# Optimization experiments

Measured on AMD Instinct MI355X. Metric: run time of the kernel, lower is better.

## Reference

```python
import jax, jax.numpy as jnp
import numpy as np
from math import sqrt


def setup_inputs() -> dict:
    key = jax.random.key(0)
    kq, kk, kv = jax.random.split(key, 3)
    B, L, S, H, E, D = 2, 4096, 4096, 8, 64, 64
    queries = jax.random.normal(kq, (B, L, H, E), dtype=jnp.float32)
    keys = jax.random.normal(kk, (B, S, H, E), dtype=jnp.float32)
    values = jax.random.normal(kv, (B, S, H, D), dtype=jnp.float32)
    attn_mask = jnp.zeros((1,), dtype=bool)  # unused (mask_flag=False)
    return {"queries": queries, "keys": keys, "values": values, "attn_mask": attn_mask}


def reference(queries, keys, values, attn_mask):
    # queries: [B,L,H,E], keys: [B,S,H,E], values: [B,S,H,D]
    E = queries.shape[-1]
    scale = 1.0 / sqrt(E)
    # log-domain value preprocessing: exp(V - max_over_seq(V))
    value_max = jnp.max(values, axis=1, keepdims=True)  # [B,1,H,D]
    v_exp = jnp.exp(values - value_max)                 # [B,S,H,D]
    # standard QK^T softmax (mask_flag=False, dropout=0 in eval)
    scores = jnp.einsum('blhe,bshe->bhls', queries, keys)  # [B,H,L,S]
    A = jax.nn.softmax(scale * scores, axis=-1)
    V = jnp.einsum('bhls,bshd->blhd', A, v_exp)            # [B,L,H,D]
    # log-domain postprocessing: log(AV) + value_max (broadcasts over L)
    V = jnp.log(V) + value_max
    return V
```

## Files before the change

kernel.cpp:

```cpp
#include <hip/hip_runtime.h>
#include <math.h>

#define NB 2
#define NL 4096
#define NS 4096
#define NH 8
#define NE 64
#define ND 64
#define SB 64
#define NT (NS / SB)
#define GT (NT / 2)
#define TILE_B 8192
#define LOG2E 1.4426950408889634f
#define SC2 (0.125f * LOG2E)

typedef __attribute__((ext_vector_type(8))) short bf16x8;
typedef __attribute__((ext_vector_type(4))) float f32x4;
typedef __attribute__((ext_vector_type(16))) float f32x16;
typedef unsigned short ushort_t;

__device__ __forceinline__ short f2bf(float f) {
  union { float f; unsigned u; } v; v.f = f;
  unsigned u = v.u;
  return (short)((u + 0x7fffu + ((u >> 16) & 1u)) >> 16);
}

__device__ __forceinline__ unsigned cvt_pk_bf16(float lo, float hi) {
  unsigned r;
  asm("v_cvt_pk_bf16_f32 %0, %1, %2" : "=v"(r) : "v"(lo), "v"(hi));
  return r;
}

__device__ __forceinline__ void gload16(const void* g, void* l) {
  __builtin_amdgcn_global_load_lds(
      (const __attribute__((address_space(1))) void*)g,
      (__attribute__((address_space(3))) void*)l, 16, 0, 0);
}


__global__ __launch_bounds__(256) void kvprep(const float* __restrict__ Kg,
                                              const float* __restrict__ Vg,
                                              ushort_t* __restrict__ kimg,
                                              ushort_t* __restrict__ vimg) {
  int blk = blockIdx.x;
  int bh = blk >> 6, tile = blk & 63;
  int b = bh >> 3, h = bh & 7;
  int t = threadIdx.x;
  int srow = t >> 2, c16 = (t & 3) * 16;
  {
    const float4* p4 =
        (const float4*)(Kg + (((size_t)b * NS + tile * SB + srow) * NH + h) * NE + c16);
    float4 a = p4[0], bq = p4[1], c = p4[2], d = p4[3];
    unsigned u0 = cvt_pk_bf16(a.x, a.y), u1 = cvt_pk_bf16(a.z, a.w);
    unsigned u2 = cvt_pk_bf16(bq.x, bq.y), u3 = cvt_pk_bf16(bq.z, bq.w);
    unsigned u4 = cvt_pk_bf16(c.x, c.y), u5 = cvt_pk_bf16(c.z, c.w);
    unsigned u6 = cvt_pk_bf16(d.x, d.y), u7 = cvt_pk_bf16(d.z, d.w);
    char* base = (char*)kimg + (size_t)blk * TILE_B;
    int off0 = (c16 >> 4) * 2048 + (srow >> 5) * 1024 + (srow & 31) * 16;
    uint4 w0 = {u0, u1, u2, u3}, w1 = {u4, u5, u6, u7};
    *(uint4*)(base + off0) = w0;
    *(uint4*)(base + off0 + 512) = w1;
  }
  {
    __shared__ short Vsh[64 * 72];
    const float4* p4 =
        (const float4*)(Vg + (((size_t)b * NS + tile * SB + srow) * NH + h) * ND + c16);
    float4 va = p4[0], vb = p4[1], vc = p4[2], vd = p4[3];
    float fv[16] = {va.x, va.y, va.z, va.w, vb.x, vb.y, vb.z, vb.w,
                    vc.x, vc.y, vc.z, vc.w, vd.x, vd.y, vd.z, vd.w};
#pragma unroll
    for (int i = 0; i < 16; ++i)
      Vsh[(c16 + i) * 72 + srow] = f2bf(__expf(fv[i]));
    __syncthreads();
    int dr = t >> 2, sc = (t & 3) * 16;
    bf16x8 o0 = *(const bf16x8*)&Vsh[dr * 72 + sc];
    bf16x8 o1 = *(const bf16x8*)&Vsh[dr * 72 + sc + 8];
    char* base = (char*)vimg + (size_t)blk * TILE_B;
    int off0 = (sc >> 4) * 2048 + (dr >> 5) * 1024 + (dr & 31) * 16;
    *(bf16x8*)(base + off0) = o0;
    *(bf16x8*)(base + off0 + 512) = o1;
  }
}

__global__ __launch_bounds__(512) void laser_fast(
    const float* __restrict__ Qg, const ushort_t* __restrict__ Kimg,
    const ushort_t* __restrict__ Vimg, float* __restrict__ Og) {
  int orig = blockIdx.x;
  int bid = (orig & 7) * 64 + (orig >> 3);
  int qt = bid & 31;
  int bh = bid >> 5;
  int b = bh >> 3, hh = bh & 7;
  int t = threadIdx.x;
  int w = t >> 6;
  int grp = w >> 2;
  int wi = w & 3;
  int lane = t & 63;
  int lq = lane & 31;
  int h = lane >> 5;

  __shared__ __attribute__((aligned(16))) char smem[65536];
  char* kls = smem + grp * 16384;
  char* vls = smem + 32768 + grp * 16384;

  const char* kbase = (const char*)Kimg + (size_t)bh * (NT * TILE_B);
  const char* vbase = (const char*)Vimg + (size_t)bh * (NT * TILE_B);

  int q0 = qt * 128 + wi * 32;
  const float* qp = Qg + (((size_t)b * NL + q0 + lq) * NH + hh) * NE;
  bf16x8 qf[4];
#pragma unroll
  for (int kk = 0; kk < 4; ++kk) {
    int e0 = 16 * kk + 8 * h;
    float4 x = *(const float4*)(qp + e0);
    float4 y = *(const float4*)(qp + e0 + 4);
    union { bf16x8 v; unsigned u[4]; } tm;
    tm.u[0] = cvt_pk_bf16(x.x * SC2, x.y * SC2);
    tm.u[1] = cvt_pk_bf16(x.z * SC2, x.w * SC2);
    tm.u[2] = cvt_pk_bf16(y.x * SC2, y.y * SC2);
    tm.u[3] = cvt_pk_bf16(y.z * SC2, y.w * SC2);
    qf[kk] = tm.v;
  }

  f32x16 acc0, acc1;
  float l_r = 0.f;
#pragma unroll
  for (int i = 0; i < 16; ++i) { acc0[i] = 0.f; acc1[i] = 0.f; }

  int soff = wi * 2048 + lane * 16;
  int tbase = grp * GT;
  int fb = h * 512 + lq * 16;

#define STAGE(buf, ti)                                                       \
  do {                                                                       \
    const char* ks = kbase + (size_t)(tbase + (ti)) * TILE_B + soff;         \
    const char* vs = vbase + (size_t)(tbase + (ti)) * TILE_B + soff;         \
    gload16(ks, kls + (buf) * 8192 + wi * 2048);                             \
    gload16(ks + 1024, kls + (buf) * 8192 + wi * 2048 + 1024);               \
    gload16(vs, vls + (buf) * 8192 + wi * 2048);                             \
    gload16(vs + 1024, vls + (buf) * 8192 + wi * 2048 + 1024);               \
  } while (0)

#define MAKE_PA(P, g, idx)                                                   \
    do {                                                                     \
      unsigned a0 = cvt_pk_bf16(P[8 * (g) + 0], P[8 * (g) + 1]);             \
      unsigned a1 = cvt_pk_bf16(P[8 * (g) + 2], P[8 * (g) + 3]);             \
      unsigned b0 = cvt_pk_bf16(P[8 * (g) + 4], P[8 * (g) + 5]);             \
      unsigned b1 = cvt_pk_bf16(P[8 * (g) + 6], P[8 * (g) + 7]);             \
      auto w02 = __builtin_amdgcn_permlane32_swap(a0, b0, false, false);     \
      auto w13 = __builtin_amdgcn_permlane32_swap(a1, b1, false, false);     \
      union { bf16x8 v; unsigned u[4]; } tm;                                 \
      tm.u[0] = w02[0]; tm.u[1] = w13[0]; tm.u[2] = w02[1]; tm.u[3] = w13[1];\
      pa[idx] = tm.v;                                                        \
    } while (0)

#define COMPUTE(curb)                                                        \
  do {                                                                       \
    const char* Kc = kls + (curb) * 8192;                                    \
    const char* Vc = vls + (curb) * 8192;                                    \
    f32x16 s0, s1;                                                           \
    _Pragma("unroll")                                                        \
    for (int i = 0; i < 16; ++i) { s0[i] = 0.f; s1[i] = 0.f; }               \
    __builtin_amdgcn_s_setprio(1);                                           \
    _Pragma("unroll")                                                        \
    for (int kk = 0; kk < 4; ++kk) {                                         \
      bf16x8 ka = *(const bf16x8*)(Kc + fb + kk * 2048);                     \
      bf16x8 kb = *(const bf16x8*)(Kc + fb + kk * 2048 + 1024);              \
      s0 = __builtin_amdgcn_mfma_f32_32x32x16_bf16(ka, qf[kk], s0, 0, 0, 0); \
      s1 = __builtin_amdgcn_mfma_f32_32x32x16_bf16(kb, qf[kk], s1, 0, 0, 0); \
    }                                                                        \
    __builtin_amdgcn_s_setprio(0);                                           \
    _Pragma("unroll")                                                        \
    for (int i = 0; i < 16; ++i) {                                           \
      s0[i] = __builtin_amdgcn_exp2f(s0[i]);                                 \
      s1[i] = __builtin_amdgcn_exp2f(s1[i]);                                 \
    }                                                                        \
    {                                                                        \
      float t0 = (s0[0] + s0[1]) + (s0[2] + s0[3]);                          \
      float t1 = (s0[4] + s0[5]) + (s0[6] + s0[7]);                          \
      float t2 = (s0[8] + s0[9]) + (s0[10] + s0[11]);                        \
      float t3 = (s0[12] + s0[13]) + (s0[14] + s0[15]);                      \
      float t4 = (s1[0] + s1[1]) + (s1[2] + s1[3]);                          \
      float t5 = (s1[4] + s1[5]) + (s1[6] + s1[7]);                          \
      float t6 = (s1[8] + s1[9]) + (s1[10] + s1[11]);                        \
      float t7 = (s1[12] + s1[13]) + (s1[14] + s1[15]);                      \
      l_r += ((t0 + t1) + (t2 + t3)) + ((t4 + t5) + (t6 + t7));              \
    }                                                                        \
    bf16x8 pa[4];                                                            \
    MAKE_PA(s0, 0, 0);                                                       \
    MAKE_PA(s0, 1, 1);                                                       \
    MAKE_PA(s1, 0, 2);                                                       \
    MAKE_PA(s1, 1, 3);                                                       \
    __builtin_amdgcn_s_setprio(1);                                           \
    _Pragma("unroll")                                                        \
    for (int kk = 0; kk < 4; ++kk) {                                         \
      bf16x8 v0 = *(const bf16x8*)(Vc + fb + kk * 2048);                     \
      bf16x8 v1 = *(const bf16x8*)(Vc + fb + kk * 2048 + 1024);              \
      acc0 = __builtin_amdgcn_mfma_f32_32x32x16_bf16(pa[kk], v0, acc0, 0, 0, 0); \
      acc1 = __builtin_amdgcn_mfma_f32_32x32x16_bf16(pa[kk], v1, acc1, 0, 0, 0); \
    }                                                                        \
    __builtin_amdgcn_s_setprio(0);                                           \
  } while (0)

  STAGE(0, 0);
  int cur = 0;
  for (int ti = 0; ti < GT - 1; ++ti) {
    STAGE(cur ^ 1, ti + 1);
    asm volatile("s_waitcnt vmcnt(4)" ::: "memory");
    __builtin_amdgcn_s_barrier();
    COMPUTE(cur);
    asm volatile("s_waitcnt lgkmcnt(0)" ::: "memory");
    __builtin_amdgcn_s_barrier();
    cur ^= 1;
  }
  asm volatile("s_waitcnt vmcnt(0)" ::: "memory");
  __builtin_amdgcn_s_barrier();
  COMPUTE(cur);
#undef STAGE
#undef MAKE_PA
#undef COMPUTE

  __syncthreads();
  float* exch = (float*)(void*)smem;
  float* lex  = (float*)(void*)(smem + 32768);
  float* lsm  = (float*)(void*)(smem + 33792);
  if (grp == 1) {
    float* e = exch + wi * 2048 + lane;
#pragma unroll
    for (int r = 0; r < 16; ++r) {
      e[r * 64] = acc0[r];
      e[(16 + r) * 64] = acc1[r];
    }
    lex[wi * 64 + lane] = l_r;
  }
  __syncthreads();
  if (grp == 0) {
    float* e = exch + wi * 2048 + lane;
#pragma unroll
    for (int r = 0; r < 16; ++r) {
      acc0[r] += e[r * 64];
      acc1[r] += e[(16 + r) * 64];
    }
    l_r += lex[wi * 64 + lane];

    union { float f; unsigned u; } cu;
    cu.f = l_r;
    auto mm = __builtin_amdgcn_permlane32_swap(cu.u, cu.u, false, false);
    union { unsigned u; float f; } m0, m1;
    m0.u = mm[0]; m1.u = mm[1];
    lsm[wi * 32 + lq] = m0.f + m1.f;

#pragma unroll
    for (int r = 0; r < 16; ++r) {
      int q = (r & 3) + 8 * (r >> 2) + 4 * h;
      float logl = __logf(lsm[wi * 32 + q]);
      size_t o = (((size_t)b * NL + q0 + q) * NH + hh) * ND + lq;
      Og[o] = __logf(acc0[r]) - logl;
      Og[o + 32] = __logf(acc1[r]) - logl;
    }
  }
}

__global__ void vmax_partial(const float* __restrict__ Vp, float* __restrict__ part) {
  int blk = blockIdx.x;
  int bh = blk >> 4, ck = blk & 15;
  int b = bh >> 3, h = bh & 7;
  int t = threadIdx.x;
  int d = t & 63, g = t >> 6;
  const float* base = Vp + (((size_t)b * NS + ck * 256) * NH + h) * ND + d;
  float m = -INFINITY;
  for (int s = g; s < 256; s += 4)
    m = fmaxf(m, base[(size_t)s * NH * ND]);
  __shared__ float red[4][64];
  red[g][d] = m;
  __syncthreads();
  if (t < 64)
    part[(size_t)blk * 64 + t] =
        fmaxf(fmaxf(red[0][t], red[1][t]), fmaxf(red[2][t], red[3][t]));
}

__global__ void vmax_reduce(const float* __restrict__ part, float* __restrict__ vmax) {
  int bh = blockIdx.x, t = threadIdx.x;
  float m = -INFINITY;
#pragma unroll
  for (int c = 0; c < 16; ++c)
    m = fmaxf(m, part[((size_t)bh * 16 + c) * 64 + t]);
  vmax[bh * 64 + t] = m;
}

__global__ __launch_bounds__(256) void laser_slow(
    const float* __restrict__ Qg, const float* __restrict__ Kg,
    const float* __restrict__ Vg, const float* __restrict__ vmax,
    float* __restrict__ Og) {
  int bid = blockIdx.x;
  int qt = bid & 63;
  int bh = bid >> 6;
  int b = bh >> 3, h = bh & 7;
  int t = threadIdx.x;
  int w = t >> 6;
  int lane = t & 63;
  int lr = lane & 15;
  int lg = lane >> 4;

  __shared__ short Kt[SB * NE];
  __shared__ short Vt[ND * SB];
  __shared__ short Pl[4][16 * SB];
  __shared__ float vmx[ND];

  if (t < ND) vmx[t] = vmax[bh * ND + t];

  int q0 = qt * 64;
  int qrow = q0 + w * 16 + lr;
  const float* qptr = Qg + (((size_t)b * NL + qrow) * NH + h) * NE;
  bf16x8 qf[2];
#pragma unroll
  for (int kf = 0; kf < 2; ++kf) {
    const float4* p4 = (const float4*)(qptr + kf * 32 + lg * 8);
    float4 a = p4[0], bq = p4[1];
    qf[kf][0] = f2bf(a.x);  qf[kf][1] = f2bf(a.y);
    qf[kf][2] = f2bf(a.z);  qf[kf][3] = f2bf(a.w);
    qf[kf][4] = f2bf(bq.x); qf[kf][5] = f2bf(bq.y);
    qf[kf][6] = f2bf(bq.z); qf[kf][7] = f2bf(bq.w);
  }

  f32x4 acc_o[4];
  float m_r[4], l_r[4];
  const f32x4 fzero = {0.f, 0.f, 0.f, 0.f};
#pragma unroll
  for (int i = 0; i < 4; ++i) { acc_o[i] = fzero; m_r[i] = -INFINITY; l_r[i] = 0.f; }

  const float scale = 0.125f;
  int srow = t >> 2;
  int c16 = (t & 3) * 16;

  for (int s0 = 0; s0 < NS; s0 += SB) {
    __syncthreads();
    {
      const float4* kp4 =
          (const float4*)(Kg + (((size_t)b * NS + (s0 + srow)) * NH + h) * NE + c16);
      float4 t0 = kp4[0], t1 = kp4[1], t2 = kp4[2], t3 = kp4[3];
      bf16x8 c0, c1;
      c0[0] = f2bf(t0.x); c0[1] = f2bf(t0.y); c0[2] = f2bf(t0.z); c0[3] = f2bf(t0.w);
      c0[4] = f2bf(t1.x); c0[5] = f2bf(t1.y); c0[6] = f2bf(t1.z); c0[7] = f2bf(t1.w);
      c1[0] = f2bf(t2.x); c1[1] = f2bf(t2.y); c1[2] = f2bf(t2.z); c1[3] = f2bf(t2.w);
      c1[4] = f2bf(t3.x); c1[5] = f2bf(t3.y); c1[6] = f2bf(t3.z); c1[7] = f2bf(t3.w);
      int base = srow * 128 + c16 * 2;
      int swz = (srow & 7) << 4;
      *(bf16x8*)((char*)Kt + ((base) ^ swz)) = c0;
      *(bf16x8*)((char*)Kt + ((base + 16) ^ swz)) = c1;
    }
    {
      const float4* vp4 =
          (const float4*)(Vg + (((size_t)b * NS + (s0 + srow)) * NH + h) * ND + c16);
      float4 t0 = vp4[0], t1 = vp4[1], t2 = vp4[2], t3 = vp4[3];
      float fv[16] = {t0.x, t0.y, t0.z, t0.w, t1.x, t1.y, t1.z, t1.w,
                      t2.x, t2.y, t2.z, t2.w, t3.x, t3.y, t3.z, t3.w};
#pragma unroll
      for (int i = 0; i < 16; ++i) {
        int d = c16 + i;
        int byte = (d * 128 + srow * 2) ^ ((d & 7) << 4);
        *(short*)((char*)Vt + byte) = f2bf(__expf(fv[i] - vmx[d]));
      }
    }
    __syncthreads();

    f32x4 sacc[4];
#pragma unroll
    for (int jt = 0; jt < 4; ++jt) sacc[jt] = fzero;
#pragma unroll
    for (int jt = 0; jt < 4; ++jt) {
      int srw = jt * 16 + lr;
      int rb = srw * 128;
      int swz = (srw & 7) << 4;
      bf16x8 kb0 = *(const bf16x8*)((const char*)Kt + ((rb + lg * 16) ^ swz));
      bf16x8 kb1 = *(const bf16x8*)((const char*)Kt + ((rb + 64 + lg * 16) ^ swz));
      sacc[jt] = __builtin_amdgcn_mfma_f32_16x16x32_bf16(qf[0], kb0, sacc[jt], 0, 0, 0);
      sacc[jt] = __builtin_amdgcn_mfma_f32_16x16x32_bf16(qf[1], kb1, sacc[jt], 0, 0, 0);
    }

    float mnew[4], corr[4];
#pragma unroll
    for (int r = 0; r < 4; ++r) {
      float x = fmaxf(fmaxf(sacc[0][r], sacc[1][r]),
                      fmaxf(sacc[2][r], sacc[3][r])) * scale;
      x = fmaxf(x, __shfl_xor(x, 1));
      x = fmaxf(x, __shfl_xor(x, 2));
      x = fmaxf(x, __shfl_xor(x, 4));
      x = fmaxf(x, __shfl_xor(x, 8));
      mnew[r] = fmaxf(m_r[r], x);
      corr[r] = __expf(m_r[r] - mnew[r]);
    }
    float rs[4] = {0.f, 0.f, 0.f, 0.f};
    short pb[4][4];
#pragma unroll
    for (int jt = 0; jt < 4; ++jt)
#pragma unroll
      for (int r = 0; r < 4; ++r) {
        float p = __expf(sacc[jt][r] * scale - mnew[r]);
        rs[r] += p;
        pb[jt][r] = f2bf(p);
      }
#pragma unroll
    for (int r = 0; r < 4; ++r) {
      float x = rs[r];
      x += __shfl_xor(x, 1);
      x += __shfl_xor(x, 2);
      x += __shfl_xor(x, 4);
      x += __shfl_xor(x, 8);
      l_r[r] = l_r[r] * corr[r] + x;
      m_r[r] = mnew[r];
    }
    short* pwv = &Pl[w][0];
#pragma unroll
    for (int jt = 0; jt < 4; ++jt)
#pragma unroll
      for (int r = 0; r < 4; ++r) {
        int row = lg * 4 + r, col = jt * 16 + lr;
        int byte = (row * 128 + col * 2) ^ ((row & 7) << 4);
        *(short*)((char*)pwv + byte) = pb[jt][r];
      }
#pragma unroll
    for (int dt = 0; dt < 4; ++dt)
#pragma unroll
      for (int r = 0; r < 4; ++r) acc_o[dt][r] *= corr[r];
#pragma unroll
    for (int kf = 0; kf < 2; ++kf) {
      int ab = lr * 128;
      int aswz = (lr & 7) << 4;
      bf16x8 pa = *(const bf16x8*)((const char*)pwv + ((ab + kf * 64 + lg * 16) ^ aswz));
#pragma unroll
      for (int dt = 0; dt < 4; ++dt) {
        int drow = dt * 16 + lr;
        int vb_byte = (drow * 128 + kf * 64 + lg * 16) ^ ((drow & 7) << 4);
        bf16x8 vb = *(const bf16x8*)((const char*)Vt + vb_byte);
        acc_o[dt] = __builtin_amdgcn_mfma_f32_16x16x32_bf16(pa, vb, acc_o[dt], 0, 0, 0);
      }
    }
  }

#pragma unroll
  for (int r = 0; r < 4; ++r) {
    int row = q0 + w * 16 + lg * 4 + r;
    float logl = __logf(l_r[r]);
#pragma unroll
    for (int dt = 0; dt < 4; ++dt) {
      int d = dt * 16 + lr;
      Og[(((size_t)b * NL + row) * NH + h) * ND + d] =
          __logf(acc_o[dt][r]) - logl + vmx[d];
    }
  }
}

extern "C" void kernel_launch(void* const* d_in, const int* in_sizes, int n_in,
                              void* d_out, int out_size, void* d_ws, size_t ws_size,
                              hipStream_t stream) {
  (void)in_sizes; (void)n_in; (void)out_size;
  const float* Q = (const float*)d_in[0];
  const float* K = (const float*)d_in[1];
  const float* V = (const float*)d_in[2];
  float* out = (float*)d_out;

  float* vmax = (float*)d_ws;
  float* part = (float*)((char*)d_ws + 4096);
  const size_t kimg_off = 1u << 20;
  const size_t vimg_off = (size_t)9u << 20;
  const size_t img_bytes = (size_t)16 * NT * TILE_B;
  bool fast = ws_size >= vimg_off + img_bytes;

  if (fast) {
    ushort_t* kimg = (ushort_t*)((char*)d_ws + kimg_off);
    ushort_t* vimg = (ushort_t*)((char*)d_ws + vimg_off);
    kvprep<<<dim3(1024), dim3(256), 0, stream>>>(K, V, kimg, vimg);
    laser_fast<<<dim3(512), dim3(512), 0, stream>>>(Q, kimg, vimg, out);
  } else {
    vmax_partial<<<dim3(256), dim3(256), 0, stream>>>(V, part);
    vmax_reduce<<<dim3(16), dim3(64), 0, stream>>>(part, vmax);
    laser_slow<<<dim3(1024), dim3(256), 0, stream>>>(Q, K, V, vmax, out);
  }
}
```

Before: 92.69 us.

## Process two 32-query tiles per wave to reuse K/V tiles across queries

Each wave now handles 64 queries instead of 32, so a block covers 256 queries and the grid shrinks from 512 to 256 blocks. K fragments are loaded into registers once and fed to two sets of QK MFMAs, and V fragments are read for both PV accumulations, halving LDS/global K/V traffic per query. This doubles the accumulator and score register footprint. With only 256 blocks on a 256-CU device, occupancy and load balance may suffer. The exchange buffer grows past 64KB of LDS, which may limit residency despite the launch_bounds hint of 2.

```diff
diff --git a/kernel.cpp b/kernel.cpp
--- a/kernel.cpp
+++ b/kernel.cpp
@@ -82,13 +82,13 @@
   }
 }
 
-__global__ __launch_bounds__(512) void laser_fast(
+__global__ __launch_bounds__(512, 2) void laser_fast(
     const float* __restrict__ Qg, const ushort_t* __restrict__ Kimg,
     const ushort_t* __restrict__ Vimg, float* __restrict__ Og) {
   int orig = blockIdx.x;
-  int bid = (orig & 7) * 64 + (orig >> 3);
-  int qt = bid & 31;
-  int bh = bid >> 5;
+  int bid = (orig & 7) * 32 + (orig >> 3);
+  int qt = bid & 15;
+  int bh = bid >> 4;
   int b = bh >> 3, hh = bh & 7;
   int t = threadIdx.x;
   int w = t >> 6;
@@ -98,33 +98,43 @@
   int lq = lane & 31;
   int h = lane >> 5;
 
-  __shared__ __attribute__((aligned(16))) char smem[65536];
+  __shared__ __attribute__((aligned(16))) char smem[68608];
   char* kls = smem + grp * 16384;
   char* vls = smem + 32768 + grp * 16384;
 
   const char* kbase = (const char*)Kimg + (size_t)bh * (NT * TILE_B);
   const char* vbase = (const char*)Vimg + (size_t)bh * (NT * TILE_B);
 
-  int q0 = qt * 128 + wi * 32;
-  const float* qp = Qg + (((size_t)b * NL + q0 + lq) * NH + hh) * NE;
-  bf16x8 qf[4];
+  int q0 = qt * 256 + wi * 64;
+  const float* qpa = Qg + (((size_t)b * NL + q0 + lq) * NH + hh) * NE;
+  const float* qpb = Qg + (((size_t)b * NL + q0 + 32 + lq) * NH + hh) * NE;
+  bf16x8 qfa[4], qfb[4];
 #pragma unroll
   for (int kk = 0; kk < 4; ++kk) {
     int e0 = 16 * kk + 8 * h;
-    float4 x = *(const float4*)(qp + e0);
-    float4 y = *(const float4*)(qp + e0 + 4);
+    float4 x = *(const float4*)(qpa + e0);
+    float4 y = *(const float4*)(qpa + e0 + 4);
     union { bf16x8 v; unsigned u[4]; } tm;
     tm.u[0] = cvt_pk_bf16(x.x * SC2, x.y * SC2);
     tm.u[1] = cvt_pk_bf16(x.z * SC2, x.w * SC2);
     tm.u[2] = cvt_pk_bf16(y.x * SC2, y.y * SC2);
     tm.u[3] = cvt_pk_bf16(y.z * SC2, y.w * SC2);
-    qf[kk] = tm.v;
-  }
-
-  f32x16 acc0, acc1;
-  float l_r = 0.f;
-#pragma unroll
-  for (int i = 0; i < 16; ++i) { acc0[i] = 0.f; acc1[i] = 0.f; }
+    qfa[kk] = tm.v;
+    float4 x2 = *(const float4*)(qpb + e0);
+    float4 y2 = *(const float4*)(qpb + e0 + 4);
+    tm.u[0] = cvt_pk_bf16(x2.x * SC2, x2.y * SC2);
+    tm.u[1] = cvt_pk_bf16(x2.z * SC2, x2.w * SC2);
+    tm.u[2] = cvt_pk_bf16(y2.x * SC2, y2.y * SC2);
+    tm.u[3] = cvt_pk_bf16(y2.z * SC2, y2.w * SC2);
+    qfb[kk] = tm.v;
+  }
+
+  f32x16 acca0, acca1, accb0, accb1;
+  float l_a = 0.f, l_b = 0.f;
+#pragma unroll
+  for (int i = 0; i < 16; ++i) {
+    acca0[i] = 0.f; acca1[i] = 0.f; accb0[i] = 0.f; accb1[i] = 0.f;
+  }
 
   int soff = wi * 2048 + lane * 16;
   int tbase = grp * GT;
@@ -140,33 +150,83 @@
     gload16(vs + 1024, vls + (buf) * 8192 + wi * 2048 + 1024);               \
   } while (0)
 
-#define MAKE_PA(P, g, idx)                                                   \
+#define MAKE_PA(P0, P1)                                                      \
     do {                                                                     \
-      unsigned a0 = cvt_pk_bf16(P[8 * (g) + 0], P[8 * (g) + 1]);             \
-      unsigned a1 = cvt_pk_bf16(P[8 * (g) + 2], P[8 * (g) + 3]);             \
-      unsigned b0 = cvt_pk_bf16(P[8 * (g) + 4], P[8 * (g) + 5]);             \
-      unsigned b1 = cvt_pk_bf16(P[8 * (g) + 6], P[8 * (g) + 7]);             \
-      auto w02 = __builtin_amdgcn_permlane32_swap(a0, b0, false, false);     \
-      auto w13 = __builtin_amdgcn_permlane32_swap(a1, b1, false, false);     \
-      union { bf16x8 v; unsigned u[4]; } tm;                                 \
-      tm.u[0] = w02[0]; tm.u[1] = w13[0]; tm.u[2] = w02[1]; tm.u[3] = w13[1];\
-      pa[idx] = tm.v;                                                        \
+      unsigned a0, a1, b0, b1;                                               \
+      a0 = cvt_pk_bf16(P0[0], P0[1]); a1 = cvt_pk_bf16(P0[2], P0[3]);        \
+      b0 = cvt_pk_bf16(P0[4], P0[5]); b1 = cvt_pk_bf16(P0[6], P0[7]);        \
+      {                                                                      \
+        auto w02 = __builtin_amdgcn_permlane32_swap(a0, b0, false, false);   \
+        auto w13 = __builtin_amdgcn_permlane32_swap(a1, b1, false, false);   \
+        union { bf16x8 v; unsigned u[4]; } tm;                               \
+        tm.u[0] = w02[0]; tm.u[1] = w13[0]; tm.u[2] = w02[1]; tm.u[3] = w13[1]; \
+        pa[0] = tm.v;                                                        \
+      }                                                                      \
+      a0 = cvt_pk_bf16(P0[8], P0[9]);   a1 = cvt_pk_bf16(P0[10], P0[11]);    \
+      b0 = cvt_pk_bf16(P0[12], P0[13]); b1 = cvt_pk_bf16(P0[14], P0[15]);    \
+      {                                                                      \
+        auto w02 = __builtin_amdgcn_permlane32_swap(a0, b0, false, false);   \
+        auto w13 = __builtin_amdgcn_permlane32_swap(a1, b1, false, false);   \
+        union { bf16x8 v; unsigned u[4]; } tm;                               \
+        tm.u[0] = w02[0]; tm.u[1] = w13[0]; tm.u[2] = w02[1]; tm.u[3] = w13[1]; \
+        pa[1] = tm.v;                                                        \
+      }                                                                      \
+      a0 = cvt_pk_bf16(P1[0], P1[1]); a1 = cvt_pk_bf16(P1[2], P1[3]);        \
+      b0 = cvt_pk_bf16(P1[4], P1[5]); b1 = cvt_pk_bf16(P1[6], P1[7]);        \
+      {                                                                      \
+        auto w02 = __builtin_amdgcn_permlane32_swap(a0, b0, false, false);   \
+        auto w13 = __builtin_amdgcn_permlane32_swap(a1, b1, false, false);   \
+        union { bf16x8 v; unsigned u[4]; } tm;                               \
+        tm.u[0] = w02[0]; tm.u[1] = w13[0]; tm.u[2] = w02[1]; tm.u[3] = w13[1]; \
+        pa[2] = tm.v;                                                        \
+      }                                                                      \
+      a0 = cvt_pk_bf16(P1[8], P1[9]);   a1 = cvt_pk_bf16(P1[10], P1[11]);    \
+      b0 = cvt_pk_bf16(P1[12], P1[13]); b1 = cvt_pk_bf16(P1[14], P1[15]);    \
+      {                                                                      \
+        auto w02 = __builtin_amdgcn_permlane32_swap(a0, b0, false, false);   \
+        auto w13 = __builtin_amdgcn_permlane32_swap(a1, b1, false, false);   \
+        union { bf16x8 v; unsigned u[4]; } tm;                               \
+        tm.u[0] = w02[0]; tm.u[1] = w13[0]; tm.u[2] = w02[1]; tm.u[3] = w13[1]; \
+        pa[3] = tm.v;                                                        \
+      }                                                                      \
+    } while (0)
+
+#define SUMTREE(dst, P0, P1)                                                 \
+    do {                                                                     \
+      float t0 = (P0[0] + P0[1]) + (P0[2] + P0[3]);                          \
+      float t1 = (P0[4] + P0[5]) + (P0[6] + P0[7]);                          \
+      float t2 = (P0[8] + P0[9]) + (P0[10] + P0[11]);                        \
+      float t3 = (P0[12] + P0[13]) + (P0[14] + P0[15]);                      \
+      float t4 = (P1[0] + P1[1]) + (P1[2] + P1[3]);                          \
+      float t5 = (P1[4] + P1[5]) + (P1[6] + P1[7]);                          \
+      float t6 = (P1[8] + P1[9]) + (P1[10] + P1[11]);                        \
+      float t7 = (P1[12] + P1[13]) + (P1[14] + P1[15]);                      \
+      dst += ((t0 + t1) + (t2 + t3)) + ((t4 + t5) + (t6 + t7));              \
     } while (0)
 
 #define COMPUTE(curb)                                                        \
   do {                                                                       \
     const char* Kc = kls + (curb) * 8192;                                    \
     const char* Vc = vls + (curb) * 8192;                                    \
-    f32x16 s0, s1;                                                           \
+    bf16x8 kf[8];                                                            \
     _Pragma("unroll")                                                        \
-    for (int i = 0; i < 16; ++i) { s0[i] = 0.f; s1[i] = 0.f; }               \
+    for (int kk = 0; kk < 4; ++kk) {                                         \
+      kf[2 * kk] = *(const bf16x8*)(Kc + fb + kk * 2048);                    \
+      kf[2 * kk + 1] = *(const bf16x8*)(Kc + fb + kk * 2048 + 1024);         \
+    }                                                                        \
+    f32x16 s0, s1, u0, u1;                                                   \
+    _Pragma("unroll")                                                        \
+    for (int i = 0; i < 16; ++i) { s0[i] = 0.f; s1[i] = 0.f; u0[i] = 0.f; u1[i] = 0.f; } \
     __builtin_amdgcn_s_setprio(1);                                           \
     _Pragma("unroll")                                                        \
     for (int kk = 0; kk < 4; ++kk) {                                         \
-      bf16x8 ka = *(const bf16x8*)(Kc + fb + kk * 2048);                     \
-      bf16x8 kb = *(const bf16x8*)(Kc + fb + kk * 2048 + 1024);              \
-      s0 = __builtin_amdgcn_mfma_f32_32x32x16_bf16(ka, qf[kk], s0, 0, 0, 0); \
-      s1 = __builtin_amdgcn_mfma_f32_32x32x16_bf16(kb, qf[kk], s1, 0, 0, 0); \
+      s0 = __builtin_amdgcn_mfma_f32_32x32x16_bf16(kf[2 * kk], qfa[kk], s0, 0, 0, 0); \
+      s1 = __builtin_amdgcn_mfma_f32_32x32x16_bf16(kf[2 * kk + 1], qfa[kk], s1, 0, 0, 0); \
+    }                                                                        \
+    _Pragma("unroll")                                                        \
+    for (int kk = 0; kk < 4; ++kk) {                                         \
+      u0 = __builtin_amdgcn_mfma_f32_32x32x16_bf16(kf[2 * kk], qfb[kk], u0, 0, 0, 0); \
+      u1 = __builtin_amdgcn_mfma_f32_32x32x16_bf16(kf[2 * kk + 1], qfb[kk], u1, 0, 0, 0); \
     }                                                                        \
     __builtin_amdgcn_s_setprio(0);                                           \
     _Pragma("unroll")                                                        \
@@ -174,31 +234,39 @@
       s0[i] = __builtin_amdgcn_exp2f(s0[i]);                                 \
       s1[i] = __builtin_amdgcn_exp2f(s1[i]);                                 \
     }                                                                        \
+    SUMTREE(l_a, s0, s1);                                                    \
     {                                                                        \
-      float t0 = (s0[0] + s0[1]) + (s0[2] + s0[3]);                          \
-      float t1 = (s0[4] + s0[5]) + (s0[6] + s0[7]);                          \
-      float t2 = (s0[8] + s0[9]) + (s0[10] + s0[11]);                        \
-      float t3 = (s0[12] + s0[13]) + (s0[14] + s0[15]);                      \
-      float t4 = (s1[0] + s1[1]) + (s1[2] + s1[3]);                          \
-      float t5 = (s1[4] + s1[5]) + (s1[6] + s1[7]);                          \
-      float t6 = (s1[8] + s1[9]) + (s1[10] + s1[11]);                        \
-      float t7 = (s1[12] + s1[13]) + (s1[14] + s1[15]);                      \
-      l_r += ((t0 + t1) + (t2 + t3)) + ((t4 + t5) + (t6 + t7));              \
-    }                                                                        \
-    bf16x8 pa[4];                                                            \
-    MAKE_PA(s0, 0, 0);                                                       \
-    MAKE_PA(s0, 1, 1);                                                       \
-    MAKE_PA(s1, 0, 2);                                                       \
-    MAKE_PA(s1, 1, 3);                                                       \
-    __builtin_amdgcn_s_setprio(1);                                           \
+      bf16x8 pa[4];                                                          \
+      MAKE_PA(s0, s1);                                                       \
+      __builtin_amdgcn_s_setprio(1);                                         \
+      _Pragma("unroll")                                                      \
+      for (int kk = 0; kk < 4; ++kk) {                                       \
+        bf16x8 v0 = *(const bf16x8*)(Vc + fb + kk * 2048);                   \
+        bf16x8 v1 = *(const bf16x8*)(Vc + fb + kk * 2048 + 1024);            \
+        acca0 = __builtin_amdgcn_mfma_f32_32x32x16_bf16(pa[kk], v0, acca0, 0, 0, 0); \
+        acca1 = __builtin_amdgcn_mfma_f32_32x32x16_bf16(pa[kk], v1, acca1, 0, 0, 0); \
+      }                                                                      \
+      __builtin_amdgcn_s_setprio(0);                                         \
+    }                                                                        \
     _Pragma("unroll")                                                        \
-    for (int kk = 0; kk < 4; ++kk) {                                         \
-      bf16x8 v0 = *(const bf16x8*)(Vc + fb + kk * 2048);                     \
-      bf16x8 v1 = *(const bf16x8*)(Vc + fb + kk * 2048 + 1024);              \
-      acc0 = __builtin_amdgcn_mfma_f32_32x32x16_bf16(pa[kk], v0, acc0, 0, 0, 0); \
-      acc1 = __builtin_amdgcn_mfma_f32_32x32x16_bf16(pa[kk], v1, acc1, 0, 0, 0); \
-    }                                                                        \
-    __builtin_amdgcn_s_setprio(0);                                           \
+    for (int i = 0; i < 16; ++i) {                                           \
+      u0[i] = __builtin_amdgcn_exp2f(u0[i]);                                 \
+      u1[i] = __builtin_amdgcn_exp2f(u1[i]);                                 \
+    }                                                                        \
+    SUMTREE(l_b, u0, u1);                                                    \
+    {                                                                        \
+      bf16x8 pa[4];                                                          \
+      MAKE_PA(u0, u1);                                                       \
+      __builtin_amdgcn_s_setprio(1);                                         \
+      _Pragma("unroll")                                                      \
+      for (int kk = 0; kk < 4; ++kk) {                                       \
+        bf16x8 v0 = *(const bf16x8*)(Vc + fb + kk * 2048);                   \
+        bf16x8 v1 = *(const bf16x8*)(Vc + fb + kk * 2048 + 1024);            \
+        accb0 = __builtin_amdgcn_mfma_f32_32x32x16_bf16(pa[kk], v0, accb0, 0, 0, 0); \
+        accb1 = __builtin_amdgcn_mfma_f32_32x32x16_bf16(pa[kk], v1, accb1, 0, 0, 0); \
+      }                                                                      \
+      __builtin_amdgcn_s_setprio(0);                                         \
+    }                                                                        \
   } while (0)
 
   STAGE(0, 0);
@@ -217,45 +285,60 @@
   COMPUTE(cur);
 #undef STAGE
 #undef MAKE_PA
+#undef SUMTREE
 #undef COMPUTE
 
   __syncthreads();
   float* exch = (float*)(void*)smem;
-  float* lex  = (float*)(void*)(smem + 32768);
-  float* lsm  = (float*)(void*)(smem + 33792);
+  float* lex  = (float*)(void*)(smem + 65536);
+  float* lsm  = (float*)(void*)(smem + 67584);
   if (grp == 1) {
-    float* e = exch + wi * 2048 + lane;
+    float* e = exch + wi * 4096 + lane;
 #pragma unroll
     for (int r = 0; r < 16; ++r) {
-      e[r * 64] = acc0[r];
-      e[(16 + r) * 64] = acc1[r];
-    }
-    lex[wi * 64 + lane] = l_r;
+      e[r * 64] = acca0[r];
+      e[(16 + r) * 64] = acca1[r];
+      e[(32 + r) * 64] = accb0[r];
+      e[(48 + r) * 64] = accb1[r];
+    }
+    lex[wi * 128 + lane] = l_a;
+    lex[wi * 128 + 64 + lane] = l_b;
   }
   __syncthreads();
   if (grp == 0) {
-    float* e = exch + wi * 2048 + lane;
+    float* e = exch + wi * 4096 + lane;
 #pragma unroll
     for (int r = 0; r < 16; ++r) {
-      acc0[r] += e[r * 64];
-      acc1[r] += e[(16 + r) * 64];
-    }
-    l_r += lex[wi * 64 + lane];
+      acca0[r] += e[r * 64];
+      acca1[r] += e[(16 + r) * 64];
+      accb0[r] += e[(32 + r) * 64];
+      accb1[r] += e[(48 + r) * 64];
+    }
+    l_a += lex[wi * 128 + lane];
+    l_b += lex[wi * 128 + 64 + lane];
 
     union { float f; unsigned u; } cu;
-    cu.f = l_r;
-    auto mm = __builtin_amdgcn_permlane32_swap(cu.u, cu.u, false, false);
-    union { unsigned u; float f; } m0, m1;
-    m0.u = mm[0]; m1.u = mm[1];
-    lsm[wi * 32 + lq] = m0.f + m1.f;
+    cu.f = l_a;
+    auto ma = __builtin_amdgcn_permlane32_swap(cu.u, cu.u, false, false);
+    union { unsigned u; float f; } x0, x1;
+    x0.u = ma[0]; x1.u = ma[1];
+    lsm[wi * 64 + lq] = x0.f + x1.f;
+    cu.f = l_b;
+    auto mb = __builtin_amdgcn_permlane32_swap(cu.u, cu.u, false, false);
+    x0.u = mb[0]; x1.u = mb[1];
+    lsm[wi * 64 + 32 + lq] = x0.f + x1.f;
 
 #pragma unroll
     for (int r = 0; r < 16; ++r) {
-      int q = (r & 3) + 8 * (r >> 2) + 4 * h;
-      float logl = __logf(lsm[wi * 32 + q]);
-      size_t o = (((size_t)b * NL + q0 + q) * NH + hh) * ND + lq;
-      Og[o] = __logf(acc0[r]) - logl;
-      Og[o + 32] = __logf(acc1[r]) - logl;
+      int cr = (r & 3) + 8 * (r >> 2) + 4 * h;
+      float logla = __logf(lsm[wi * 64 + cr]);
+      float loglb = __logf(lsm[wi * 64 + 32 + cr]);
+      size_t oa = (((size_t)b * NL + q0 + cr) * NH + hh) * ND + lq;
+      size_t ob = (((size_t)b * NL + q0 + 32 + cr) * NH + hh) * ND + lq;
+      Og[oa] = __logf(acca0[r]) - logla;
+      Og[oa + 32] = __logf(acca1[r]) - logla;
+      Og[ob] = __logf(accb0[r]) - loglb;
+      Og[ob + 32] = __logf(accb1[r]) - loglb;
     }
   }
 }
@@ -470,7 +553,7 @@
     ushort_t* kimg = (ushort_t*)((char*)d_ws + kimg_off);
     ushort_t* vimg = (ushort_t*)((char*)d_ws + vimg_off);
     kvprep<<<dim3(1024), dim3(256), 0, stream>>>(K, V, kimg, vimg);
-    laser_fast<<<dim3(512), dim3(512), 0, stream>>>(Q, kimg, vimg, out);
+    laser_fast<<<dim3(256), dim3(512), 0, stream>>>(Q, kimg, vimg, out);
   } else {
     vmax_partial<<<dim3(256), dim3(256), 0, stream>>>(V, part);
     vmax_reduce<<<dim3(16), dim3(64), 0, stream>>>(part, vmax);
```

After: 91.57 us. About the same (-1.2%).
